# Performance work log

Measured on AMD Instinct MI355X. Metric: run time of the kernel, lower is better.

Reference implementation:

```python
import jax, jax.numpy as jnp
import numpy as np

BETA = 0.25
K = 1024   # codebook_size
D = 64     # emb_dim


def setup_inputs() -> dict:
    key = jax.random.key(0)
    k1, k2 = jax.random.split(key)
    z_e = jax.random.normal(k1, (32, 64, 64, D), dtype=jnp.float32)
    codebook = jax.random.normal(k2, (K, D), dtype=jnp.float32) * 0.05
    return {"z_e": z_e, "codebook": codebook}


def reference(z_e, codebook):
    sg = jax.lax.stop_gradient
    k, d = codebook.shape
    z = z_e.reshape(-1, d)                                   # [N, D]
    # squared euclidean distances: ||z||^2 + ||e||^2 - 2 z.e
    z_sq = jnp.sum(z * z, axis=1, keepdims=True)             # [N, 1]
    e_sq = jnp.sum(codebook * codebook, axis=1)              # [K]
    distances = z_sq + e_sq[None, :] - 2.0 * (z @ codebook.T)  # [N, K]
    indices = jnp.argmin(distances, axis=1)                  # [N] int
    z_q = jnp.take(codebook, indices, axis=0).reshape(z_e.shape)
    commitment = jnp.mean((sg(z_e) - z_q) ** 2)
    codebook_loss = jnp.mean((z_e - sg(z_q)) ** 2)
    z_q_st = z_e + sg(z_q - z_e)
    loss_vq = codebook_loss + BETA * commitment
    # perplexity (no-grad in original)
    n = z.shape[0]
    counts = jnp.zeros((k,), dtype=jnp.float32).at[indices].add(1.0)
    avg_probs = sg(counts / n)
    perplexity = jnp.exp(-jnp.sum(avg_probs * jnp.log(avg_probs + 1e-12)))
    return z_q_st, indices.reshape(z_e.shape[:-1]), loss_vq, perplexity
```

## Files before the change

### kernel.cpp

```cpp
#include <hip/hip_runtime.h>

#define N_VEC   131072
#define D       64
#define KCODES  1024
#define NT      64
#define BLK     256
#define VPB     128
#define CH      4
#define NCH     (NT / CH)

typedef __attribute__((ext_vector_type(8))) short bf16x8;
typedef __attribute__((ext_vector_type(4))) float f32x4;

#define GLD16(dst, src) __builtin_amdgcn_global_load_lds(                      \
    (const __attribute__((address_space(1))) void*)(src),                      \
    (__attribute__((address_space(3))) void*)(dst), 16, 0, 0)


__device__ __forceinline__ float4 f4fma(float4 a, float4 b, float4 c) {
    return make_float4(fmaf(a.x, b.x, c.x), fmaf(a.y, b.y, c.y),
                       fmaf(a.z, b.z, c.z), fmaf(a.w, b.w, c.w));
}
__device__ __forceinline__ float f4rsum(float4 a) {
    return (a.x + a.y) + (a.z + a.w);
}
__device__ __forceinline__ unsigned short f2bf(float f) {
    union { float f; unsigned u; } x; x.f = f;
    unsigned r = x.u + 0x7FFFu + ((x.u >> 16) & 1u);
    return (unsigned short)(r >> 16);
}
__device__ __forceinline__ float bf2f(unsigned short h) {
    union { unsigned u; float f; } x; x.u = ((unsigned)h) << 16;
    return x.f;
}
__device__ __forceinline__ int   f_as_i(float f) { union { float f; int i; } x; x.f = f; return x.i; }
__device__ __forceinline__ float i_as_f(int i)   { union { int i; float f; } x; x.i = i; return x.f; }

__global__ void prep_kernel(const float* __restrict__ cb, float* __restrict__ esq,
                            bf16x8* __restrict__ afrag, float4* __restrict__ efrag) {
    __shared__ float sesq[64];
    const int tid = threadIdx.x;
    const int c0  = blockIdx.x * 64;
    if (tid < 64) {
        const float4* c4 = reinterpret_cast<const float4*>(cb + (size_t)(c0 + tid) * D);
        float4 p = make_float4(0.f, 0.f, 0.f, 0.f);
        #pragma unroll
        for (int i = 0; i < 16; ++i) { float4 v = c4[i]; p = f4fma(v, v, p); }
        float e = f4rsum(p);
        esq[c0 + tid] = e;
        sesq[tid] = e;
    }
    __syncthreads();
    const int tt = tid >> 6;
    const int L  = tid & 63;
    const int t  = blockIdx.x * 4 + tt;
    const int g  = L >> 4;
    const int r  = t * 16 + (L & 15);
    #pragma unroll
    for (int ks = 0; ks < 2; ++ks) {
        const float* src = cb + (size_t)r * D + ks * 32 + g * 8;
        bf16x8 h, l;
        #pragma unroll
        for (int e = 0; e < 8; ++e) {
            float f = src[e];
            unsigned short hb = f2bf(f);
            float lo = f - bf2f(hb);
            h[e] = (short)hb;
            l[e] = (short)f2bf(lo);
        }
        afrag[(t * 4 + ks * 2 + 0) * 64 + L] = h;
        afrag[(t * 4 + ks * 2 + 1) * 64 + L] = l;
    }
    float4 ef;
    ef.x = -0.5f * sesq[tt * 16 + g * 4 + 0];
    ef.y = -0.5f * sesq[tt * 16 + g * 4 + 1];
    ef.z = -0.5f * sesq[tt * 16 + g * 4 + 2];
    ef.w = -0.5f * sesq[tt * 16 + g * 4 + 3];
    efrag[t * 64 + L] = ef;
}

__device__ __forceinline__ void insd(float ov, int og,
                                     float& v0, float& v1, float& v2,
                                     int& g0, int& g1, int& g2) {
    bool b1 = (ov > v0) || (ov == v0 && og < g0);
    bool b2 = (ov > v1) || (ov == v1 && og < g1);
    bool b3 = (ov > v2) || (ov == v2 && og < g2);
    float nv2 = b2 ? v1 : (b3 ? ov : v2);
    int   ng2 = b2 ? g1 : (b3 ? og : g2);
    float nv1 = b1 ? v0 : (b2 ? ov : v1);
    int   ng1 = b1 ? g0 : (b2 ? og : g1);
    v0 = b1 ? ov : v0;
    g0 = b1 ? og : g0;
    v1 = nv1; g1 = ng1; v2 = nv2; g2 = ng2;
}

__launch_bounds__(BLK)
__global__ void vq_fused(const float* __restrict__ z_e, const float* __restrict__ cb,
                         const float* __restrict__ esq,
                         const float4* __restrict__ afrag4, const float4* __restrict__ efrag,
                         float* __restrict__ zq_out, float* __restrict__ idx_out,
                         float* __restrict__ sse, int* __restrict__ counts) {
    __shared__ float4 scb[2][CH * 4 * 64];
    char* ovl = (char*)&scb[0][0];
    int  (*scand)[3] = reinterpret_cast<int(*)[3]>(ovl);
    float* sZsq = reinterpret_cast<float*>(ovl + 2048);
    float* sS1  = reinterpret_cast<float*>(ovl + 2560);
    float* sS2  = reinterpret_cast<float*>(ovl + 3072);
    float* sC2  = reinterpret_cast<float*>(ovl + 3584);
    float* sred = reinterpret_cast<float*>(ovl + 4096);

    const int tid  = threadIdx.x;
    const int wave = tid >> 6;
    const int L    = tid & 63;
    const int lrow = L & 15;
    const int g    = L >> 4;
    const size_t vbase = (size_t)blockIdx.x * VPB + wave * 32;

    bf16x8 zhi[2][2], zlo[2][2];
    #pragma unroll
    for (int b = 0; b < 2; ++b) {
        #pragma unroll
        for (int ks = 0; ks < 2; ++ks) {
            const float* zp = z_e + (vbase + b * 16 + lrow) * D + ks * 32 + g * 8;
            float4 u0 = *reinterpret_cast<const float4*>(zp);
            float4 u1 = *reinterpret_cast<const float4*>(zp + 4);
            float fv[8] = {u0.x, u0.y, u0.z, u0.w, u1.x, u1.y, u1.z, u1.w};
            bf16x8 h, l;
            #pragma unroll
            for (int e = 0; e < 8; ++e) {
                unsigned short hb = f2bf(fv[e]);
                float lo = fv[e] - bf2f(hb);
                h[e] = (short)hb;
                l[e] = (short)f2bf(lo);
            }
            zhi[b][ks] = h; zlo[b][ks] = l;
        }
    }

    float m1[2], m2[2], m3[2];
    #pragma unroll
    for (int b = 0; b < 2; ++b) { m1[b] = m2[b] = m3[b] = -INFINITY; }

    #pragma unroll
    for (int i = 0; i < 4; ++i) GLD16(&scb[0][i * BLK + tid], afrag4 + i * BLK + tid);

    int cur = 0;
    for (int c = 0; c < NCH; ++c) {
        __syncthreads();
        if (c + 1 < NCH) {
            const float4* gA = afrag4 + (size_t)(c + 1) * (CH * 4 * 64);
            #pragma unroll
            for (int i = 0; i < 4; ++i) GLD16(&scb[cur ^ 1][i * BLK + tid], gA + i * BLK + tid);
        }

        #pragma unroll
        for (int tt = 0; tt < CH; ++tt) {
            const int t = c * CH + tt;
            const bf16x8* fr = reinterpret_cast<const bf16x8*>(&scb[cur][tt * 256]);
            bf16x8 Ah0 = fr[0 * 64 + L];
            bf16x8 Al0 = fr[1 * 64 + L];
            bf16x8 Ah1 = fr[2 * 64 + L];
            bf16x8 Al1 = fr[3 * 64 + L];
            f32x4 einit;
            {
                float4 ef = efrag[t * 64 + L];
                einit[0] = ef.x; einit[1] = ef.y; einit[2] = ef.z; einit[3] = ef.w;
            }

            #pragma unroll
            for (int b = 0; b < 2; ++b) {
                f32x4 aA = (f32x4){0.f, 0.f, 0.f, 0.f};
                aA = __builtin_amdgcn_mfma_f32_16x16x32_bf16(Ah0, zhi[b][0], aA, 0, 0, 0);
                f32x4 aB = __builtin_amdgcn_mfma_f32_16x16x32_bf16(Ah0, zlo[b][0], einit, 0, 0, 0);
                aA = __builtin_amdgcn_mfma_f32_16x16x32_bf16(Ah1, zhi[b][1], aA, 0, 0, 0);
                aB = __builtin_amdgcn_mfma_f32_16x16x32_bf16(Ah1, zlo[b][1], aB, 0, 0, 0);
                aA = __builtin_amdgcn_mfma_f32_16x16x32_bf16(Al0, zhi[b][0], aA, 0, 0, 0);
                aB = __builtin_amdgcn_mfma_f32_16x16x32_bf16(Al1, zhi[b][1], aB, 0, 0, 0);

                #pragma unroll
                for (int j = 0; j < 4; ++j) {
                    float r = aA[j] + aB[j];
                    int komp = 255 - ((t << 2) | j);
                    float pd = i_as_f((f_as_i(r) & 0xFFFFFF00) | komp);
                    float mn = fminf(m2[b], pd);
                    float md = __builtin_amdgcn_fmed3f(m1[b], pd, m2[b]);
                    m1[b] = fmaxf(m1[b], pd);
                    m2[b] = md;
                    m3[b] = fmaxf(m3[b], mn);
                }
            }
        }
        cur ^= 1;
    }

    __syncthreads();

    #pragma unroll
    for (int b = 0; b < 2; ++b) {
        float v0, v1, v2; int g0, g1, g2;
        {
            int p0 = f_as_i(m1[b]), p1 = f_as_i(m2[b]), p2 = f_as_i(m3[b]);
            int c0 = 255 - (p0 & 255), c1 = 255 - (p1 & 255), c2 = 255 - (p2 & 255);
            v0 = i_as_f(p0 & ~255); g0 = (c0 >> 2) * 16 + g * 4 + (c0 & 3);
            v1 = i_as_f(p1 & ~255); g1 = (c1 >> 2) * 16 + g * 4 + (c1 & 3);
            v2 = i_as_f(p2 & ~255); g2 = (c2 >> 2) * 16 + g * 4 + (c2 & 3);
        }
        #pragma unroll
        for (int m = 16; m <= 32; m <<= 1) {
            float ov0 = __shfl_xor(v0, m), ov1 = __shfl_xor(v1, m), ov2 = __shfl_xor(v2, m);
            int   og0 = __shfl_xor(g0, m), og1 = __shfl_xor(g1, m), og2 = __shfl_xor(g2, m);
            insd(ov0, og0, v0, v1, v2, g0, g1, g2);
            insd(ov1, og1, v0, v1, v2, g0, g1, g2);
            insd(ov2, og2, v0, v1, v2, g0, g1, g2);
        }
        if (g == 0) {
            int lv = wave * 32 + b * 16 + lrow;
            scand[lv][0] = g0; scand[lv][1] = g1; scand[lv][2] = g2;
        }
    }
    __syncthreads();

    const int vid = tid & (VPB - 1);
    const int sub = tid >> 7;
    const size_t n = (size_t)blockIdx.x * VPB + vid;
    {
        const float4* z4 = reinterpret_cast<const float4*>(z_e + n * D);
        if (sub == 0) {
            int ci0 = scand[vid][0];
            const float4* cp0 = reinterpret_cast<const float4*>(cb + (size_t)ci0 * D);
            float4 pq = make_float4(0.f, 0.f, 0.f, 0.f);
            float4 s0 = pq;
            #pragma unroll
            for (int i = 0; i < 16; ++i) {
                float4 zz = z4[i];
                pq = f4fma(zz, zz, pq);
                s0 = f4fma(zz, cp0[i], s0);
            }
            sZsq[vid] = f4rsum(pq);
            sS1[vid]  = f4rsum(s0);
        } else {
            int ci1 = scand[vid][1];
            int ci2 = scand[vid][2];
            const float4* cp1 = reinterpret_cast<const float4*>(cb + (size_t)ci1 * D);
            const float4* cp2 = reinterpret_cast<const float4*>(cb + (size_t)ci2 * D);
            float4 s1 = make_float4(0.f, 0.f, 0.f, 0.f);
            float4 s2 = s1;
            #pragma unroll
            for (int i = 0; i < 16; ++i) {
                float4 zz = z4[i];
                s1 = f4fma(zz, cp1[i], s1);
                s2 = f4fma(zz, cp2[i], s2);
            }
            sS2[vid] = f4rsum(s1);
            sC2[vid] = f4rsum(s2);
        }
    }
    __syncthreads();

    float v = 0.f;
    if (sub == 0) {
        int ci0 = scand[vid][0], ci1 = scand[vid][1], ci2 = scand[vid][2];
        float zsq = sZsq[vid];
        float d0 = fmaf(-2.0f, sS1[vid], zsq + esq[ci0]);
        float d1 = fmaf(-2.0f, sS2[vid], zsq + esq[ci1]);
        float d2 = fmaf(-2.0f, sC2[vid], zsq + esq[ci2]);
        float bd = d0; int bi = ci0;
        if (d1 < bd || (d1 == bd && ci1 < bi)) { bd = d1; bi = ci1; }
        if (d2 < bd || (d2 == bd && ci2 < bi)) { bd = d2; bi = ci2; }
        idx_out[n] = (float)bi;
        atomicAdd(&counts[bi], 1);
        scand[vid][0] = bi;
        v = bd;
    }
    #pragma unroll
    for (int off = 32; off > 0; off >>= 1) v += __shfl_down(v, off);
    if ((tid & 63) == 0) sred[tid >> 6] = v;
    __syncthreads();
    if (tid == 0) atomicAdd(sse, (sred[0] + sred[1]) + (sred[2] + sred[3]));

    const float4* cb4 = reinterpret_cast<const float4*>(cb);
    float4* zq4 = reinterpret_cast<float4*>(zq_out) + (size_t)blockIdx.x * (VPB * 16);
    #pragma unroll
    for (int i = 0; i < 8; ++i) {
        int mi  = i * BLK + tid;
        int vec = mi >> 4;
        int e   = mi & 15;
        zq4[mi] = cb4[(size_t)scand[vec][0] * 16 + e];
    }
}

__global__ void finalize_kernel(const int* __restrict__ counts, const float* __restrict__ sse,
                                float* __restrict__ out_loss, float* __restrict__ out_perp) {
    __shared__ float red[256];
    int tid = threadIdx.x;
    float hsum = 0.f;
    for (int k = tid; k < KCODES; k += 256) {
        float p = (float)counts[k] / (float)N_VEC;
        hsum += p * logf(p + 1e-12f);
    }
    red[tid] = hsum;
    __syncthreads();
    for (int s = 128; s > 0; s >>= 1) {
        if (tid < s) red[tid] += red[tid + s];
        __syncthreads();
    }
    if (tid == 0) {
        out_loss[0] = 1.25f * sse[0] / 8388608.0f;
        out_perp[0] = expf(-red[0]);
    }
}

extern "C" void kernel_launch(void* const* d_in, const int* in_sizes, int n_in,
                              void* d_out, int out_size, void* d_ws, size_t ws_size,
                              hipStream_t stream) {
    const float* z_e = (const float*)d_in[0];
    const float* cb  = (const float*)d_in[1];

    float* out  = (float*)d_out;
    float* zq   = out;
    float* idxo = out + (size_t)N_VEC * D;
    float* loss = idxo + N_VEC;
    float* perp = loss + 1;

    char* ws = (char*)d_ws;
    int*    counts = (int*)ws;
    float*  sse    = (float*)(ws + 4096);
    float*  esq    = (float*)(ws + 5120);
    float4* efrag  = (float4*)(ws + 16384);
    bf16x8* afrag  = (bf16x8*)(ws + 81920);

    hipMemsetAsync(d_ws, 0, 5120, stream);
    prep_kernel<<<16, 256, 0, stream>>>(cb, esq, afrag, efrag);
    vq_fused<<<N_VEC / VPB, BLK, 0, stream>>>(z_e, cb, esq, (const float4*)afrag, efrag,
                                              zq, idxo, sse, counts);
    finalize_kernel<<<1, 256, 0, stream>>>(counts, sse, loss, perp);
}
```

Measured before the change: 123.2 us.

## Stage codebook norm fragments through LDS and restructure distance accumulation

The per-tile codebook norm fragment now arrives by async global-to-LDS loads, double-buffered alongside the A fragments, instead of a global read inside the hot loop. The norm is no longer preloaded into the MFMA accumulator; the score is formed afterwards as 2*(hi + lo parts) minus the norm. The MFMA chains are rebalanced between the two accumulators, and the top-3 update becomes a min/max cascade. This adds extra FMAs and a little LDS traffic per tile, and the changed rounding of the score could alter near-tie candidate ordering.

New measurement: 106.0 us. -14.0%, faster.

```diff
diff --git a/kernel.cpp b/kernel.cpp
--- a/kernel.cpp
+++ b/kernel.cpp
@@ -72,10 +72,10 @@
         afrag[(t * 4 + ks * 2 + 1) * 64 + L] = l;
     }
     float4 ef;
-    ef.x = -0.5f * sesq[tt * 16 + g * 4 + 0];
-    ef.y = -0.5f * sesq[tt * 16 + g * 4 + 1];
-    ef.z = -0.5f * sesq[tt * 16 + g * 4 + 2];
-    ef.w = -0.5f * sesq[tt * 16 + g * 4 + 3];
+    ef.x = sesq[tt * 16 + g * 4 + 0];
+    ef.y = sesq[tt * 16 + g * 4 + 1];
+    ef.z = sesq[tt * 16 + g * 4 + 2];
+    ef.w = sesq[tt * 16 + g * 4 + 3];
     efrag[t * 64 + L] = ef;
 }
 
@@ -101,6 +101,7 @@
                          float* __restrict__ zq_out, float* __restrict__ idx_out,
                          float* __restrict__ sse, int* __restrict__ counts) {
     __shared__ float4 scb[2][CH * 4 * 64];
+    __shared__ float4 sef[2][CH * 64];
     char* ovl = (char*)&scb[0][0];
     int  (*scand)[3] = reinterpret_cast<int(*)[3]>(ovl);
     float* sZsq = reinterpret_cast<float*>(ovl + 2048);
@@ -143,50 +144,49 @@
 
     #pragma unroll
     for (int i = 0; i < 4; ++i) GLD16(&scb[0][i * BLK + tid], afrag4 + i * BLK + tid);
+    GLD16(&sef[0][tid], efrag + tid);
 
     int cur = 0;
     for (int c = 0; c < NCH; ++c) {
         __syncthreads();
         if (c + 1 < NCH) {
             const float4* gA = afrag4 + (size_t)(c + 1) * (CH * 4 * 64);
+            const float4* gE = efrag + (size_t)(c + 1) * (CH * 64);
             #pragma unroll
             for (int i = 0; i < 4; ++i) GLD16(&scb[cur ^ 1][i * BLK + tid], gA + i * BLK + tid);
+            GLD16(&sef[cur ^ 1][tid], gE + tid);
         }
 
         #pragma unroll
         for (int tt = 0; tt < CH; ++tt) {
-            const int t = c * CH + tt;
+            const int tglob = c * CH + tt;
             const bf16x8* fr = reinterpret_cast<const bf16x8*>(&scb[cur][tt * 256]);
             bf16x8 Ah0 = fr[0 * 64 + L];
             bf16x8 Al0 = fr[1 * 64 + L];
             bf16x8 Ah1 = fr[2 * 64 + L];
             bf16x8 Al1 = fr[3 * 64 + L];
-            f32x4 einit;
-            {
-                float4 ef = efrag[t * 64 + L];
-                einit[0] = ef.x; einit[1] = ef.y; einit[2] = ef.z; einit[3] = ef.w;
-            }
+            float4 ef  = sef[cur][tt * 64 + L];
 
             #pragma unroll
             for (int b = 0; b < 2; ++b) {
                 f32x4 aA = (f32x4){0.f, 0.f, 0.f, 0.f};
+                f32x4 aB = (f32x4){0.f, 0.f, 0.f, 0.f};
                 aA = __builtin_amdgcn_mfma_f32_16x16x32_bf16(Ah0, zhi[b][0], aA, 0, 0, 0);
-                f32x4 aB = __builtin_amdgcn_mfma_f32_16x16x32_bf16(Ah0, zlo[b][0], einit, 0, 0, 0);
+                aB = __builtin_amdgcn_mfma_f32_16x16x32_bf16(Ah0, zlo[b][0], aB, 0, 0, 0);
+                aB = __builtin_amdgcn_mfma_f32_16x16x32_bf16(Al0, zhi[b][0], aB, 0, 0, 0);
                 aA = __builtin_amdgcn_mfma_f32_16x16x32_bf16(Ah1, zhi[b][1], aA, 0, 0, 0);
                 aB = __builtin_amdgcn_mfma_f32_16x16x32_bf16(Ah1, zlo[b][1], aB, 0, 0, 0);
-                aA = __builtin_amdgcn_mfma_f32_16x16x32_bf16(Al0, zhi[b][0], aA, 0, 0, 0);
                 aB = __builtin_amdgcn_mfma_f32_16x16x32_bf16(Al1, zhi[b][1], aB, 0, 0, 0);
 
                 #pragma unroll
                 for (int j = 0; j < 4; ++j) {
-                    float r = aA[j] + aB[j];
-                    int komp = 255 - ((t << 2) | j);
-                    float pd = i_as_f((f_as_i(r) & 0xFFFFFF00) | komp);
-                    float mn = fminf(m2[b], pd);
-                    float md = __builtin_amdgcn_fmed3f(m1[b], pd, m2[b]);
-                    m1[b] = fmaxf(m1[b], pd);
-                    m2[b] = md;
-                    m3[b] = fmaxf(m3[b], mn);
+                    float ej = (j == 0) ? ef.x : (j == 1) ? ef.y : (j == 2) ? ef.z : ef.w;
+                    float s = fmaf(2.0f, aA[j], fmaf(2.0f, aB[j], -ej));
+                    int komp = 255 - ((tglob << 2) | j);
+                    float pd = i_as_f((f_as_i(s) & 0xFFFFFF00) | komp);
+                    float t1 = fminf(m1[b], pd); m1[b] = fmaxf(m1[b], pd);
+                    float t2 = fminf(m2[b], t1); m2[b] = fmaxf(m2[b], t1);
+                    m3[b] = fmaxf(m3[b], t2);
                 }
             }
         }
```
